# Optimization experiments

Hardware: AMD Instinct MI355X
Metric: run time of the kernel (lower is better)

Reference implementation:

```python
import jax, jax.numpy as jnp
import numpy as np

B, H, S, DK, DV = 4, 16, 2048, 64, 64

def setup_inputs() -> dict:
    key = jax.random.key(0)
    k1, k2, k3, k4 = jax.random.split(key, 4)
    Q = jax.random.normal(k1, (B, H, S, DK), dtype=jnp.float32)
    K = jax.random.normal(k2, (B, H, S, DK), dtype=jnp.float32)
    V = jax.random.normal(k3, (B, H, S, DV), dtype=jnp.float32)
    mask_out = jax.random.randint(k4, (B, 1, 1, S), 0, 2).astype(jnp.bool_)
    return {"Q": Q, "K": K, "V": V, "mask_out": mask_out}

def reference(Q, K, V, mask_out):
    key_size = Q.shape[-1]
    seq_q, seq_k = Q.shape[-2], K.shape[-2]
    scale = jnp.sqrt(jnp.float32(key_size))
    # scores: [B, H, Sq, Sk]
    scores = jnp.einsum('bhqd,bhkd->bhqk', Q, K) / scale
    scores = jnp.where(mask_out, jnp.float32(-1e9), scores)
    attn = jax.nn.softmax(scores, axis=-1)
    # Gaussian relative-position decay: exp(-|i-j|^2 / (Sk^2 / 2))
    idx_q = jnp.arange(seq_q, dtype=jnp.float32)[:, None]
    idx_k = jnp.arange(seq_k, dtype=jnp.float32)[None, :]
    rel = idx_q - idx_k  # [Sq, Sk]
    decay = jnp.exp(-(rel * rel) * (2.0 / (seq_k * seq_k)))  # [Sq, Sk]
    attn = attn * decay  # broadcast over [B, H]
    return jnp.einsum('bhqk,bhkv->bhqv', attn, V)
```

## Files before the change

kernel.cpp:

```cpp
#include <hip/hip_runtime.h>
#include <hip/hip_bf16.h>

typedef __attribute__((ext_vector_type(8))) short bf16x8;
typedef __attribute__((ext_vector_type(4))) short bf16x4;
typedef __attribute__((ext_vector_type(4))) float f32x4;
typedef __attribute__((ext_vector_type(4))) unsigned u32x4;
typedef __attribute__((ext_vector_type(4))) int i32x4;

constexpr int Bn = 4, Hn = 16, S = 2048, D = 64;
constexpr int BQ = 128;
constexpr float LOG2E = 1.44269504088896340736f;

__device__ __forceinline__ unsigned cvtpk(float lo, float hi) {
    unsigned r;
    asm("v_cvt_pk_bf16_f32 %0, %1, %2" : "=v"(r) : "v"(lo), "v"(hi));
    return r;
}

__device__ __forceinline__ f32x4 mfma16(bf16x4 a, bf16x4 b, f32x4 c) {
#if __has_builtin(__builtin_amdgcn_mfma_f32_16x16x16bf16_1k)
    return __builtin_amdgcn_mfma_f32_16x16x16bf16_1k(a, b, c, 0, 0, 0);
#else
    asm volatile("v_mfma_f32_16x16x16_bf16 %0, %1, %2, %0"
                 : "+v"(c) : "v"(a), "v"(b));
    return c;
#endif
}

__global__ void compact_mask(const void* __restrict__ maskg,
                             int* __restrict__ idxp, int* __restrict__ Mg) {
    const int b = blockIdx.x, t = threadIdx.x;
    __shared__ int wsum[4];
    __shared__ int Msh;

    const unsigned* mu = (const unsigned*)maskg;
    bool is_bytes = false;
    #pragma unroll 8
    for (int i = 0; i < 64; ++i) is_bytes |= (mu[i] > 1u);

    int keep[8]; int cnt = 0;
    #pragma unroll
    for (int i = 0; i < 8; ++i) {
        const int key = t * 8 + i;
        int m;
        if (is_bytes) m = ((const unsigned char*)maskg)[b * S + key];
        else          m = ((const int*)maskg)[b * S + key];
        keep[i] = (m == 0);
        cnt += keep[i];
    }
    const int l = t & 63, w = t >> 6;
    int pre = cnt;
    #pragma unroll
    for (int d = 1; d < 64; d <<= 1) {
        int v = __shfl_up(pre, d, 64);
        if (l >= d) pre += v;
    }
    if (l == 63) wsum[w] = pre;
    __syncthreads();
    int base = 0;
    for (int i = 0; i < w; ++i) base += wsum[i];
    int offs = base + pre - cnt;
    #pragma unroll
    for (int i = 0; i < 8; ++i)
        if (keep[i]) idxp[b * S + (offs++)] = t * 8 + i;
    if (t == 255) Msh = base + pre;
    __syncthreads();
    const int M = Msh;
    for (int i = M + t; i < S; i += 256) idxp[b * S + i] = 0;
    if (M == 0)
        for (int i = t; i < S; i += 256) idxp[b * S + i] = i;
    if (t == 0) Mg[b] = (M == 0) ? -1 : M;
}

__global__ void pack_kv(const float* __restrict__ Kg, const float* __restrict__ Vg,
                        const int* __restrict__ idxp, const int* __restrict__ Mg,
                        short* __restrict__ Kw, short* __restrict__ Vw) {
    const int bh = blockIdx.x, b = bh >> 4;
    const int ck0 = blockIdx.y * 256;
    const int t = threadIdx.x;
    const int Mraw = Mg[b];
    const int M = (Mraw < 0) ? S : Mraw;
    if (ck0 >= M) return;
    const int* idxb = idxp + b * S;
    const float* Kp = Kg + (size_t)bh * S * D;
    const float* Vp = Vg + (size_t)bh * S * D;

    {
        const int dc = (t & 7) * 8;
        #pragma unroll
        for (int tile = 0; tile < 4; ++tile)
            #pragma unroll
            for (int it = 0; it < 2; ++it) {
                const int key = ck0 + tile * 64 + (t >> 3) + it * 32;
                u32x4 pk = u32x4{0u, 0u, 0u, 0u};
                if (key < M) {
                    const float* src = Kp + (size_t)idxb[key] * D + dc;
                    #pragma unroll
                    for (int jj = 0; jj < 4; ++jj)
                        pk[jj] = cvtpk(src[2 * jj], src[2 * jj + 1]);
                }
                *(u32x4*)(Kw + ((size_t)bh * S + key) * D + dc) = pk;
            }
    }
    {
        const int dv = t & 63;
        const int kb = (t >> 6) * 16;
        #pragma unroll
        for (int tile = 0; tile < 4; ++tile) {
            const int tg = (ck0 >> 6) + tile;
            float f[16];
            #pragma unroll
            for (int i = 0; i < 16; ++i) {
                const int key = ck0 + tile * 64 + kb + i;
                float v = 0.f;
                if (key < M) {
                    int row = idxb[key];
                    row = __builtin_amdgcn_readfirstlane(row);
                    v = Vp[(size_t)row * D + dv];
                }
                f[i] = v;
            }
            u32x4 p0, p1;
            #pragma unroll
            for (int jj = 0; jj < 4; ++jj) {
                p0[jj] = cvtpk(f[2 * jj], f[2 * jj + 1]);
                p1[jj] = cvtpk(f[8 + 2 * jj], f[9 + 2 * jj]);
            }
            short* dst = Vw + (((size_t)bh * 32 + tg) * 64 + dv) * 64 + kb;
            *(u32x4*)dst = p0;
            *(u32x4*)(dst + 8) = p1;
        }
    }
}

__global__ __launch_bounds__(256, 3) void attn_packed(
    const float* __restrict__ Qg, const short* __restrict__ Kw,
    const short* __restrict__ Vw, const int* __restrict__ idxp,
    const int* __restrict__ Mg, float* __restrict__ outg)
{
    __shared__ alignas(16) short Kt[2][64][64];
    __shared__ alignas(16) short Vt[2][64][64];
    __shared__ alignas(16) float dtab[2176];
    __shared__ alignas(16) int   idxs[2][64];

    const int bid  = blockIdx.x;
    const int lblk = ((bid & 7) << 7) | (bid >> 3);
    const int qt   = lblk & 15;
    const int bh   = lblk >> 4;
    const int b    = bh >> 4;
    const int q0   = qt * BQ;

    const float* Qp   = Qg + ((size_t)bh * S + q0) * D;
    const short* Ksrc = Kw + (size_t)bh * S * D;
    const short* Vsrc = Vw + (size_t)bh * 32 * 64 * 64;
    float*       Op   = outg + ((size_t)bh * S + q0) * D;
    const int*   idxb = idxp + b * S;

    const int t  = threadIdx.x;
    const int w  = t >> 6;
    const int l  = t & 63;
    const int lr = l & 15;
    const int lg = l >> 4;
    const int lx = lr & 7;

    const int  Mraw    = Mg[b];
    const bool uniform = (Mraw < 0);
    const int  M       = uniform ? S : Mraw;
    const int  ntiles  = (M + 63) >> 6;

    u32x4 kr0, kr1, vr0, vr1;
    int ir = 0;
    kr0 = *(const u32x4*)(Ksrc + t * 16);
    kr1 = *(const u32x4*)(Ksrc + t * 16 + 8);
    vr0 = *(const u32x4*)(Vsrc + t * 16);
    vr1 = *(const u32x4*)(Vsrc + t * 16 + 8);
    if (t < 64) ir = idxb[t];

    const float CD2 = (2.0f / ((float)S * (float)S)) * LOG2E;
    for (int i = t; i < 2176; i += 256) {
        const float r = (float)(q0 + i - 2047);
        dtab[i] = __builtin_exp2f(-CD2 * r * r);
    }

    const float qscale = uniform ? 0.0f : 0.125f * LOG2E;
    bf16x8 qf[2][2];
    #pragma unroll
    for (int rt = 0; rt < 2; ++rt) {
        const int row = w * 32 + rt * 16 + lr;
        #pragma unroll
        for (int g = 0; g < 2; ++g) {
            const float* src = Qp + row * D + g * 32 + lg * 8;
            union { unsigned u[4]; bf16x8 v; } cv;
            #pragma unroll
            for (int jj = 0; jj < 4; ++jj)
                cv.u[jj] = cvtpk(src[2 * jj] * qscale, src[2 * jj + 1] * qscale);
            qf[rt][g] = cv.v;
        }
    }

    f32x4 Oacc[2][4];
    #pragma unroll
    for (int rt = 0; rt < 2; ++rt)
        #pragma unroll
        for (int dt = 0; dt < 4; ++dt) Oacc[rt][dt] = f32x4{0.f, 0.f, 0.f, 0.f};
    float lrun[2] = {0.f, 0.f};

    const int qrl2047 = w * 32 + lr + 2047;

    const int srow = t >> 2;
    const int sb0  = srow * 128 + (((2 * (t & 3)) ^ (srow & 7)) << 4);

    {
        char* kd = (char*)&Kt[0][0][0];
        char* vd = (char*)&Vt[0][0][0];
        *(u32x4*)(kd + sb0)        = kr0;
        *(u32x4*)(kd + (sb0 ^ 16)) = kr1;
        *(u32x4*)(vd + sb0)        = vr0;
        *(u32x4*)(vd + (sb0 ^ 16)) = vr1;
        if (t < 64) idxs[0][t] = ir;
    }
    __syncthreads();

    int c = 0;
    for (int tt = 0; tt < ntiles; ++tt) {
        const int  rem      = M - tt * 64;
        const bool last     = (rem <= 64);
        const bool havenext = (tt + 1 < ntiles);

        if (havenext) {
            const short* kp = Ksrc + (size_t)(tt + 1) * 4096;
            const short* vp = Vsrc + (size_t)(tt + 1) * 4096;
            kr0 = *(const u32x4*)(kp + t * 16);
            kr1 = *(const u32x4*)(kp + t * 16 + 8);
            vr0 = *(const u32x4*)(vp + t * 16);
            vr1 = *(const u32x4*)(vp + t * 16 + 8);
            if (t < 64) ir = idxb[(tt + 1) * 64 + t];
        }

        const char* kbase = (const char*)&Kt[c][0][0];
        const char* vbase = (const char*)&Vt[c][0][0];

        bf16x8 kf[4][2];
        #pragma unroll
        for (int kt = 0; kt < 4; ++kt)
            #pragma unroll
            for (int g = 0; g < 2; ++g)
                kf[kt][g] = *(const bf16x8*)(kbase + (kt * 16 + lr) * 128
                                             + (((4 * g + lg) ^ lx) << 4));

        bf16x4 Xb[2][4];
        #pragma unroll
        for (int rt = 0; rt < 2; ++rt) {
            f32x4 sc[4];
            __builtin_amdgcn_s_setprio(1);
            #pragma unroll
            for (int kt = 0; kt < 4; ++kt) {
                f32x4 acc = f32x4{0.f, 0.f, 0.f, 0.f};
                acc = __builtin_amdgcn_mfma_f32_16x16x32_bf16(kf[kt][0], qf[rt][0], acc, 0, 0, 0);
                acc = __builtin_amdgcn_mfma_f32_16x16x32_bf16(kf[kt][1], qf[rt][1], acc, 0, 0, 0);
                sc[kt] = acc;
            }
            __builtin_amdgcn_s_setprio(0);
            const int qi = qrl2047 + rt * 16;
            float lp = 0.f;
            #pragma unroll
            for (int kt = 0; kt < 4; ++kt) {
                const i32x4 iv = *(const i32x4*)&idxs[c][kt * 16 + lg * 4];
                float p0 = __builtin_exp2f(sc[kt][0] - 16.0f);
                float p1 = __builtin_exp2f(sc[kt][1] - 16.0f);
                float p2 = __builtin_exp2f(sc[kt][2] - 16.0f);
                float p3 = __builtin_exp2f(sc[kt][3] - 16.0f);
                if (last) {
                    const int ck = kt * 16 + lg * 4;
                    p0 = (ck + 0 < rem) ? p0 : 0.f;
                    p1 = (ck + 1 < rem) ? p1 : 0.f;
                    p2 = (ck + 2 < rem) ? p2 : 0.f;
                    p3 = (ck + 3 < rem) ? p3 : 0.f;
                }
                lp += (p0 + p1) + (p2 + p3);
                const float d0 = dtab[qi - iv[0]];
                const float d1 = dtab[qi - iv[1]];
                const float d2 = dtab[qi - iv[2]];
                const float d3 = dtab[qi - iv[3]];
                union { unsigned u[2]; bf16x4 v; } cx;
                cx.u[0] = cvtpk(p0 * d0, p1 * d1);
                cx.u[1] = cvtpk(p2 * d2, p3 * d3);
                Xb[rt][kt] = cx.v;
            }
            lrun[rt] += lp;
        }

        __builtin_amdgcn_s_setprio(1);
        #pragma unroll
        for (int kt = 0; kt < 4; ++kt) {
            bf16x4 vA[4];
            #pragma unroll
            for (int dt = 0; dt < 4; ++dt)
                vA[dt] = *(const bf16x4*)(vbase + (dt * 16 + lr) * 128
                          + ((((2 * kt + (lg >> 1)) ^ lx) << 4) | ((lg & 1) << 3)));
            #pragma unroll
            for (int dt = 0; dt < 4; ++dt) {
                Oacc[0][dt] = mfma16(vA[dt], Xb[0][kt], Oacc[0][dt]);
                Oacc[1][dt] = mfma16(vA[dt], Xb[1][kt], Oacc[1][dt]);
            }
        }
        __builtin_amdgcn_s_setprio(0);

        if (havenext) {
            char* kd = (char*)&Kt[c ^ 1][0][0];
            char* vd = (char*)&Vt[c ^ 1][0][0];
            *(u32x4*)(kd + sb0)        = kr0;
            *(u32x4*)(kd + (sb0 ^ 16)) = kr1;
            *(u32x4*)(vd + sb0)        = vr0;
            *(u32x4*)(vd + (sb0 ^ 16)) = vr1;
            if (t < 64) idxs[c ^ 1][t] = ir;
        }
        __syncthreads();
        c ^= 1;
    }

    #pragma unroll
    for (int rt = 0; rt < 2; ++rt) {
        float ls = lrun[rt];
        ls += __shfl_xor(ls, 16, 64);
        ls += __shfl_xor(ls, 32, 64);
        const float inv = 1.0f / ls;
        const int row = w * 32 + rt * 16 + lr;
        #pragma unroll
        for (int dt = 0; dt < 4; ++dt) {
            f32x4 o = Oacc[rt][dt];
            o[0] *= inv; o[1] *= inv; o[2] *= inv; o[3] *= inv;
            *(f32x4*)&Op[(size_t)row * D + dt * 16 + lg * 4] = o;
        }
    }
}

__global__ __launch_bounds__(256, 3) void attn_gather(
    const float* __restrict__ Qg, const float* __restrict__ Kg,
    const float* __restrict__ Vg, const int* __restrict__ idxp,
    const int* __restrict__ Mg, float* __restrict__ outg)
{
    __shared__ alignas(16) short Kt[64][72];
    __shared__ alignas(16) short Vt[64][72];
    __shared__ alignas(16) float dtab[2176];
    __shared__ alignas(16) int   idxs[64];

    const int blk = blockIdx.x;
    const int qt  = blk & 15;
    const int bh  = blk >> 4;
    const int b   = bh >> 4;
    const int q0  = qt * BQ;

    const float* Qp = Qg + ((size_t)bh * S + q0) * D;
    const float* Kp = Kg + (size_t)bh * S * D;
    const float* Vp = Vg + (size_t)bh * S * D;
    float*       Op = outg + ((size_t)bh * S + q0) * D;
    const int*   idxb = idxp + b * S;

    const int t  = threadIdx.x;
    const int w  = t >> 6;
    const int l  = t & 63;
    const int lr = l & 15;
    const int lg = l >> 4;

    const int  Mraw    = Mg[b];
    const bool uniform = (Mraw < 0);
    const int  M       = uniform ? S : Mraw;

    const float CD2 = (2.0f / ((float)S * (float)S)) * LOG2E;
    for (int i = t; i < 2176; i += 256) {
        const float r = (float)(q0 + i - 2047);
        dtab[i] = __builtin_exp2f(-CD2 * r * r);
    }

    const float qscale = uniform ? 0.0f : 0.125f * LOG2E;
    bf16x8 qf[2][2];
    #pragma unroll
    for (int rt = 0; rt < 2; ++rt) {
        const int row = w * 32 + rt * 16 + lr;
        #pragma unroll
        for (int g = 0; g < 2; ++g) {
            const float* src = Qp + row * D + g * 32 + lg * 8;
            union { unsigned u[4]; bf16x8 v; } cv;
            #pragma unroll
            for (int jj = 0; jj < 4; ++jj)
                cv.u[jj] = cvtpk(src[2 * jj] * qscale, src[2 * jj + 1] * qscale);
            qf[rt][g] = cv.v;
        }
    }

    f32x4 Oacc[2][4];
    #pragma unroll
    for (int rt = 0; rt < 2; ++rt)
        #pragma unroll
        for (int dt = 0; dt < 4; ++dt) Oacc[rt][dt] = f32x4{0.f, 0.f, 0.f, 0.f};
    float lrun[2] = {0.f, 0.f};

    const int qrl2047 = w * 32 + lr + 2047;

    for (int kv = 0; kv < M; kv += 64) {
        const int  rem  = M - kv;
        const bool last = (rem <= 64);
        __syncthreads();
        {
            const int key = t >> 3;
            const int dc  = (t & 7) * 8;
            #pragma unroll
            for (int it = 0; it < 2; ++it) {
                const int row = idxb[kv + key + it * 32];
                const float* src = Kp + (size_t)row * D + dc;
                u32x4 pk;
                #pragma unroll
                for (int jj = 0; jj < 4; ++jj)
                    pk[jj] = cvtpk(src[2 * jj], src[2 * jj + 1]);
                *(u32x4*)&Kt[key + it * 32][dc] = pk;
            }
        }
        if (t < 64) idxs[t] = idxb[kv + t];
        {
            const int dv = t & 63;
            const int kb = (t >> 6) * 16;
            float f[16];
            #pragma unroll
            for (int i = 0; i < 16; ++i) {
                int row = idxb[kv + kb + i];
                row = __builtin_amdgcn_readfirstlane(row);
                f[i] = Vp[(size_t)row * D + dv];
            }
            u32x4 p0, p1;
            #pragma unroll
            for (int jj = 0; jj < 4; ++jj) {
                p0[jj] = cvtpk(f[2 * jj], f[2 * jj + 1]);
                p1[jj] = cvtpk(f[8 + 2 * jj], f[9 + 2 * jj]);
            }
            *(u32x4*)&Vt[dv][kb]     = p0;
            *(u32x4*)&Vt[dv][kb + 8] = p1;
        }
        __syncthreads();

        bf16x8 kf[4][2];
        #pragma unroll
        for (int kt = 0; kt < 4; ++kt)
            #pragma unroll
            for (int g = 0; g < 2; ++g)
                kf[kt][g] = *(const bf16x8*)&Kt[kt * 16 + lr][g * 32 + lg * 8];

        bf16x4 Xb[2][4];
        #pragma unroll
        for (int rt = 0; rt < 2; ++rt) {
            f32x4 sc[4];
            #pragma unroll
            for (int kt = 0; kt < 4; ++kt) {
                f32x4 acc = f32x4{0.f, 0.f, 0.f, 0.f};
                acc = __builtin_amdgcn_mfma_f32_16x16x32_bf16(kf[kt][0], qf[rt][0], acc, 0, 0, 0);
                acc = __builtin_amdgcn_mfma_f32_16x16x32_bf16(kf[kt][1], qf[rt][1], acc, 0, 0, 0);
                sc[kt] = acc;
            }
            const int qi = qrl2047 + rt * 16;
            float lp = 0.f;
            #pragma unroll
            for (int kt = 0; kt < 4; ++kt) {
                const i32x4 iv = *(const i32x4*)&idxs[kt * 16 + lg * 4];
                float p0 = __builtin_exp2f(sc[kt][0] - 16.0f);
                float p1 = __builtin_exp2f(sc[kt][1] - 16.0f);
                float p2 = __builtin_exp2f(sc[kt][2] - 16.0f);
                float p3 = __builtin_exp2f(sc[kt][3] - 16.0f);
                if (last) {
                    const int ck = kt * 16 + lg * 4;
                    p0 = (ck + 0 < rem) ? p0 : 0.f;
                    p1 = (ck + 1 < rem) ? p1 : 0.f;
                    p2 = (ck + 2 < rem) ? p2 : 0.f;
                    p3 = (ck + 3 < rem) ? p3 : 0.f;
                }
                lp += (p0 + p1) + (p2 + p3);
                const float d0 = dtab[qi - iv[0]];
                const float d1 = dtab[qi - iv[1]];
                const float d2 = dtab[qi - iv[2]];
                const float d3 = dtab[qi - iv[3]];
                union { unsigned u[2]; bf16x4 v; } cx;
                cx.u[0] = cvtpk(p0 * d0, p1 * d1);
                cx.u[1] = cvtpk(p2 * d2, p3 * d3);
                Xb[rt][kt] = cx.v;
            }
            lrun[rt] += lp;
        }

        #pragma unroll
        for (int kt = 0; kt < 4; ++kt) {
            bf16x4 vA[4];
            #pragma unroll
            for (int dt = 0; dt < 4; ++dt)
                vA[dt] = *(const bf16x4*)&Vt[dt * 16 + lr][kt * 16 + lg * 4];
            #pragma unroll
            for (int dt = 0; dt < 4; ++dt) {
                Oacc[0][dt] = mfma16(vA[dt], Xb[0][kt], Oacc[0][dt]);
                Oacc[1][dt] = mfma16(vA[dt], Xb[1][kt], Oacc[1][dt]);
            }
        }
    }

    #pragma unroll
    for (int rt = 0; rt < 2; ++rt) {
        float ls = lrun[rt];
        ls += __shfl_xor(ls, 16, 64);
        ls += __shfl_xor(ls, 32, 64);
        const float inv = 1.0f / ls;
        const int row = w * 32 + rt * 16 + lr;
        #pragma unroll
        for (int dt = 0; dt < 4; ++dt) {
            f32x4 o = Oacc[rt][dt];
            o[0] *= inv; o[1] *= inv; o[2] *= inv; o[3] *= inv;
            *(f32x4*)&Op[(size_t)row * D + dt * 16 + lg * 4] = o;
        }
    }
}

extern "C" void kernel_launch(void* const* d_in, const int* in_sizes, int n_in,
                              void* d_out, int out_size, void* d_ws, size_t ws_size,
                              hipStream_t stream) {
    const float* Q = (const float*)d_in[0];
    const float* K = (const float*)d_in[1];
    const float* V = (const float*)d_in[2];
    const void*  M = d_in[3];
    float* out = (float*)d_out;

    int* idxp = (int*)d_ws;
    int* Mg   = idxp + Bn * S;
    size_t base = (((size_t)(Bn * S + Bn) * 4) + 255) & ~(size_t)255;
    short* Kw = (short*)((char*)d_ws + base);
    short* Vw = Kw + (size_t)Bn * Hn * S * D;
    const size_t need = base + 2 * (size_t)Bn * Hn * S * D * sizeof(short);

    compact_mask<<<dim3(Bn), dim3(256), 0, stream>>>(M, idxp, Mg);
    const int nblk = Bn * Hn * (S / BQ);
    if (ws_size >= need) {
        pack_kv<<<dim3(Bn * Hn, S / 256), dim3(256), 0, stream>>>(K, V, idxp, Mg, Kw, Vw);
        attn_packed<<<dim3(nblk), dim3(256), 0, stream>>>(Q, Kw, Vw, idxp, Mg, out);
    } else {
        attn_gather<<<dim3(nblk), dim3(256), 0, stream>>>(Q, K, V, idxp, Mg, out);
    }
}
```

Baseline: 132.6 us.

## Split attention block into 8 waves with 16 query rows each

The packed attention kernel now runs 512 threads per block instead of 256. Each wave handles 16 query rows rather than 32, and each thread stages one 16-byte chunk of K and V per tile instead of two. This is meant to raise wave-level parallelism and cut per-thread register pressure so more waves can hide latency. In exchange, each K/V tile held in LDS is reused across fewer rows per wave, and each wave reads the K fragments once per 16 rows rather than once per 32, so LDS read traffic per useful MFMA goes up.

```diff
diff --git a/kernel.cpp b/kernel.cpp
--- a/kernel.cpp
+++ b/kernel.cpp
@@ -133,7 +133,7 @@
     }
 }
 
-__global__ __launch_bounds__(256, 3) void attn_packed(
+__global__ __launch_bounds__(512, 4) void attn_packed(
     const float* __restrict__ Qg, const short* __restrict__ Kw,
     const short* __restrict__ Vw, const int* __restrict__ idxp,
     const int* __restrict__ Mg, float* __restrict__ outg)
@@ -168,25 +168,22 @@
     const int  M       = uniform ? S : Mraw;
     const int  ntiles  = (M + 63) >> 6;
 
-    u32x4 kr0, kr1, vr0, vr1;
+    u32x4 kr, vr;
     int ir = 0;
-    kr0 = *(const u32x4*)(Ksrc + t * 16);
-    kr1 = *(const u32x4*)(Ksrc + t * 16 + 8);
-    vr0 = *(const u32x4*)(Vsrc + t * 16);
-    vr1 = *(const u32x4*)(Vsrc + t * 16 + 8);
+    kr = *(const u32x4*)(Ksrc + t * 8);
+    vr = *(const u32x4*)(Vsrc + t * 8);
     if (t < 64) ir = idxb[t];
 
     const float CD2 = (2.0f / ((float)S * (float)S)) * LOG2E;
-    for (int i = t; i < 2176; i += 256) {
+    for (int i = t; i < 2176; i += 512) {
         const float r = (float)(q0 + i - 2047);
         dtab[i] = __builtin_exp2f(-CD2 * r * r);
     }
 
     const float qscale = uniform ? 0.0f : 0.125f * LOG2E;
-    bf16x8 qf[2][2];
-    #pragma unroll
-    for (int rt = 0; rt < 2; ++rt) {
-        const int row = w * 32 + rt * 16 + lr;
+    bf16x8 qf[2];
+    {
+        const int row = w * 16 + lr;
         #pragma unroll
         for (int g = 0; g < 2; ++g) {
             const float* src = Qp + row * D + g * 32 + lg * 8;
@@ -194,31 +191,23 @@
             #pragma unroll
             for (int jj = 0; jj < 4; ++jj)
                 cv.u[jj] = cvtpk(src[2 * jj] * qscale, src[2 * jj + 1] * qscale);
-            qf[rt][g] = cv.v;
-        }
-    }
-
-    f32x4 Oacc[2][4];
-    #pragma unroll
-    for (int rt = 0; rt < 2; ++rt)
-        #pragma unroll
-        for (int dt = 0; dt < 4; ++dt) Oacc[rt][dt] = f32x4{0.f, 0.f, 0.f, 0.f};
-    float lrun[2] = {0.f, 0.f};
-
-    const int qrl2047 = w * 32 + lr + 2047;
-
-    const int srow = t >> 2;
-    const int sb0  = srow * 128 + (((2 * (t & 3)) ^ (srow & 7)) << 4);
-
-    {
-        char* kd = (char*)&Kt[0][0][0];
-        char* vd = (char*)&Vt[0][0][0];
-        *(u32x4*)(kd + sb0)        = kr0;
-        *(u32x4*)(kd + (sb0 ^ 16)) = kr1;
-        *(u32x4*)(vd + sb0)        = vr0;
-        *(u32x4*)(vd + (sb0 ^ 16)) = vr1;
-        if (t < 64) idxs[0][t] = ir;
-    }
+            qf[g] = cv.v;
+        }
+    }
+
+    f32x4 Oacc[4];
+    #pragma unroll
+    for (int dt = 0; dt < 4; ++dt) Oacc[dt] = f32x4{0.f, 0.f, 0.f, 0.f};
+    float lrun = 0.f;
+
+    const int qi = w * 16 + lr + 2047;
+
+    const int srow = t >> 3;
+    const int sb0  = srow * 128 + ((((t & 7)) ^ (srow & 7)) << 4);
+
+    *(u32x4*)((char*)&Kt[0][0][0] + sb0) = kr;
+    *(u32x4*)((char*)&Vt[0][0][0] + sb0) = vr;
+    if (t < 64) idxs[0][t] = ir;
     __syncthreads();
 
     int c = 0;
@@ -228,12 +217,8 @@
         const bool havenext = (tt + 1 < ntiles);
 
         if (havenext) {
-            const short* kp = Ksrc + (size_t)(tt + 1) * 4096;
-            const short* vp = Vsrc + (size_t)(tt + 1) * 4096;
-            kr0 = *(const u32x4*)(kp + t * 16);
-            kr1 = *(const u32x4*)(kp + t * 16 + 8);
-            vr0 = *(const u32x4*)(vp + t * 16);
-            vr1 = *(const u32x4*)(vp + t * 16 + 8);
+            kr = *(const u32x4*)(Ksrc + (size_t)(tt + 1) * 4096 + t * 8);
+            vr = *(const u32x4*)(Vsrc + (size_t)(tt + 1) * 4096 + t * 8);
             if (t < 64) ir = idxb[(tt + 1) * 64 + t];
         }
 
@@ -248,47 +233,44 @@
                 kf[kt][g] = *(const bf16x8*)(kbase + (kt * 16 + lr) * 128
                                              + (((4 * g + lg) ^ lx) << 4));
 
-        bf16x4 Xb[2][4];
-        #pragma unroll
-        for (int rt = 0; rt < 2; ++rt) {
-            f32x4 sc[4];
-            __builtin_amdgcn_s_setprio(1);
-            #pragma unroll
-            for (int kt = 0; kt < 4; ++kt) {
-                f32x4 acc = f32x4{0.f, 0.f, 0.f, 0.f};
-                acc = __builtin_amdgcn_mfma_f32_16x16x32_bf16(kf[kt][0], qf[rt][0], acc, 0, 0, 0);
-                acc = __builtin_amdgcn_mfma_f32_16x16x32_bf16(kf[kt][1], qf[rt][1], acc, 0, 0, 0);
-                sc[kt] = acc;
-            }
-            __builtin_amdgcn_s_setprio(0);
-            const int qi = qrl2047 + rt * 16;
-            float lp = 0.f;
-            #pragma unroll
-            for (int kt = 0; kt < 4; ++kt) {
-                const i32x4 iv = *(const i32x4*)&idxs[c][kt * 16 + lg * 4];
-                float p0 = __builtin_exp2f(sc[kt][0] - 16.0f);
-                float p1 = __builtin_exp2f(sc[kt][1] - 16.0f);
-                float p2 = __builtin_exp2f(sc[kt][2] - 16.0f);
-                float p3 = __builtin_exp2f(sc[kt][3] - 16.0f);
-                if (last) {
-                    const int ck = kt * 16 + lg * 4;
-                    p0 = (ck + 0 < rem) ? p0 : 0.f;
-                    p1 = (ck + 1 < rem) ? p1 : 0.f;
-                    p2 = (ck + 2 < rem) ? p2 : 0.f;
-                    p3 = (ck + 3 < rem) ? p3 : 0.f;
-                }
-                lp += (p0 + p1) + (p2 + p3);
-                const float d0 = dtab[qi - iv[0]];
-                const float d1 = dtab[qi - iv[1]];
-                const float d2 = dtab[qi - iv[2]];
-                const float d3 = dtab[qi - iv[3]];
-                union { unsigned u[2]; bf16x4 v; } cx;
-                cx.u[0] = cvtpk(p0 * d0, p1 * d1);
-                cx.u[1] = cvtpk(p2 * d2, p3 * d3);
-                Xb[rt][kt] = cx.v;
-            }
-            lrun[rt] += lp;
-        }
+        f32x4 sc[4];
+        __builtin_amdgcn_s_setprio(1);
+        #pragma unroll
+        for (int kt = 0; kt < 4; ++kt) {
+            f32x4 acc = f32x4{0.f, 0.f, 0.f, 0.f};
+            acc = __builtin_amdgcn_mfma_f32_16x16x32_bf16(kf[kt][0], qf[0], acc, 0, 0, 0);
+            acc = __builtin_amdgcn_mfma_f32_16x16x32_bf16(kf[kt][1], qf[1], acc, 0, 0, 0);
+            sc[kt] = acc;
+        }
+        __builtin_amdgcn_s_setprio(0);
+
+        bf16x4 Xb[4];
+        float lp = 0.f;
+        #pragma unroll
+        for (int kt = 0; kt < 4; ++kt) {
+            const i32x4 iv = *(const i32x4*)&idxs[c][kt * 16 + lg * 4];
+            float p0 = __builtin_exp2f(sc[kt][0] - 16.0f);
+            float p1 = __builtin_exp2f(sc[kt][1] - 16.0f);
+            float p2 = __builtin_exp2f(sc[kt][2] - 16.0f);
+            float p3 = __builtin_exp2f(sc[kt][3] - 16.0f);
+            if (last) {
+                const int ck = kt * 16 + lg * 4;
+                p0 = (ck + 0 < rem) ? p0 : 0.f;
+                p1 = (ck + 1 < rem) ? p1 : 0.f;
+                p2 = (ck + 2 < rem) ? p2 : 0.f;
+                p3 = (ck + 3 < rem) ? p3 : 0.f;
+            }
+            lp += (p0 + p1) + (p2 + p3);
+            const float d0 = dtab[qi - iv[0]];
+            const float d1 = dtab[qi - iv[1]];
+            const float d2 = dtab[qi - iv[2]];
+            const float d3 = dtab[qi - iv[3]];
+            union { unsigned u[2]; bf16x4 v; } cx;
+            cx.u[0] = cvtpk(p0 * d0, p1 * d1);
+            cx.u[1] = cvtpk(p2 * d2, p3 * d3);
+            Xb[kt] = cx.v;
+        }
+        lrun += lp;
 
         __builtin_amdgcn_s_setprio(1);
         #pragma unroll
@@ -299,36 +281,29 @@
                 vA[dt] = *(const bf16x4*)(vbase + (dt * 16 + lr) * 128
                           + ((((2 * kt + (lg >> 1)) ^ lx) << 4) | ((lg & 1) << 3)));
             #pragma unroll
-            for (int dt = 0; dt < 4; ++dt) {
-                Oacc[0][dt] = mfma16(vA[dt], Xb[0][kt], Oacc[0][dt]);
-                Oacc[1][dt] = mfma16(vA[dt], Xb[1][kt], Oacc[1][dt]);
-            }
+            for (int dt = 0; dt < 4; ++dt)
+                Oacc[dt] = mfma16(vA[dt], Xb[kt], Oacc[dt]);
         }
         __builtin_amdgcn_s_setprio(0);
 
         if (havenext) {
-            char* kd = (char*)&Kt[c ^ 1][0][0];
-            char* vd = (char*)&Vt[c ^ 1][0][0];
-            *(u32x4*)(kd + sb0)        = kr0;
-            *(u32x4*)(kd + (sb0 ^ 16)) = kr1;
-            *(u32x4*)(vd + sb0)        = vr0;
-            *(u32x4*)(vd + (sb0 ^ 16)) = vr1;
+            *(u32x4*)((char*)&Kt[c ^ 1][0][0] + sb0) = kr;
+            *(u32x4*)((char*)&Vt[c ^ 1][0][0] + sb0) = vr;
             if (t < 64) idxs[c ^ 1][t] = ir;
         }
         __syncthreads();
         c ^= 1;
     }
 
-    #pragma unroll
-    for (int rt = 0; rt < 2; ++rt) {
-        float ls = lrun[rt];
+    {
+        float ls = lrun;
         ls += __shfl_xor(ls, 16, 64);
         ls += __shfl_xor(ls, 32, 64);
         const float inv = 1.0f / ls;
-        const int row = w * 32 + rt * 16 + lr;
+        const int row = w * 16 + lr;
         #pragma unroll
         for (int dt = 0; dt < 4; ++dt) {
-            f32x4 o = Oacc[rt][dt];
+            f32x4 o = Oacc[dt];
             o[0] *= inv; o[1] *= inv; o[2] *= inv; o[3] *= inv;
             *(f32x4*)&Op[(size_t)row * D + dt * 16 + lg * 4] = o;
         }
@@ -535,7 +510,7 @@
     const int nblk = Bn * Hn * (S / BQ);
     if (ws_size >= need) {
         pack_kv<<<dim3(Bn * Hn, S / 256), dim3(256), 0, stream>>>(K, V, idxp, Mg, Kw, Vw);
-        attn_packed<<<dim3(nblk), dim3(256), 0, stream>>>(Q, Kw, Vw, idxp, Mg, out);
+        attn_packed<<<dim3(nblk), dim3(512), 0, stream>>>(Q, Kw, Vw, idxp, Mg, out);
     } else {
         attn_gather<<<dim3(nblk), dim3(256), 0, stream>>>(Q, K, V, idxp, Mg, out);
     }
```

Measured after the change: 119.7 us. -9.7%, faster.
